# Kernel tuning notes

Hardware: AMD Instinct MI355X
Metric: run time of the kernel (lower is better)

## Reference

```python
import jax, jax.numpy as jnp
import numpy as np

RADIUS = 0.2
K = 32  # num_neighbors


def ball_query(centers, points, radius, k):
    """centers [B,3,M], points [B,3,N] -> int32 indices [B,M,k].
    Matches PointNet++ CUDA semantics: first k points (in original order)
    with squared distance < radius^2; slots beyond the count are filled
    with the first valid index (0 if no point is in the ball)."""
    cn = jnp.sum(centers * centers, axis=1)              # [B,M]
    pn = jnp.sum(points * points, axis=1)                # [B,N]
    cross = jnp.einsum('bdm,bdn->bmn', centers, points)  # [B,M,N]
    d2 = cn[:, :, None] + pn[:, None, :] - 2.0 * cross   # [B,M,N]
    valid = d2 < radius * radius
    # stable argsort puts valid indices first, preserving original order
    order = jnp.argsort(jnp.logical_not(valid), axis=-1, stable=True)
    idx = order[..., :k]                                  # [B,M,k]
    count = jnp.sum(valid, axis=-1, keepdims=True)        # [B,M,1]
    fill = idx[..., :1]                                   # first valid (or 0)
    return jnp.where(jnp.arange(k)[None, None, :] < count, idx, fill)


def group(features, idx):
    """features [B,C,N], idx [B,M,K] -> [B,C,M,K]."""
    return jax.vmap(lambda f, i: jnp.take(f, i, axis=1))(features, idx)


def setup_inputs() -> dict:
    key = jax.random.key(0)
    k1, k2, k3, k4 = jax.random.split(key, 4)
    B, N, M, C, CT = 8, 8192, 2048, 64, 64
    return {
        'points_coords': jax.random.uniform(k1, (B, 3, N), dtype=jnp.float32),
        'centers_coords': jax.random.uniform(k2, (B, 3, M), dtype=jnp.float32),
        'temb': jax.random.normal(k3, (B, CT, N), dtype=jnp.float32),
        'points_features': jax.random.normal(k4, (B, C, N), dtype=jnp.float32),
    }


def reference(points_coords, centers_coords, temb, points_features):
    idx = ball_query(centers_coords, points_coords, RADIUS, K)           # [B,M,K]
    neighbor_coords = group(points_coords, idx) - centers_coords[:, :, :, None]  # [B,3,M,K]
    neighbor_features = jnp.concatenate(
        [neighbor_coords, group(points_features, idx)], axis=1)          # [B,3+C,M,K]
    temb_grouped = group(temb, idx)                                      # [B,CT,M,K]
    return neighbor_features, temb_grouped
```

## Files before the change

kernel.cpp:

```cpp
#include <hip/hip_runtime.h>

#define B  8
#define N  8192
#define M  2048
#define C  64
#define CT 64
#define K  32
#define R2 0.04f

__device__ __forceinline__ float rfl(float x) {
    union { float f; int i; } u;
    u.f = x;
    u.i = __builtin_amdgcn_readfirstlane(u.i);
    return u.f;
}

__global__ __launch_bounds__(256) void transpose_kernel(
    const float* __restrict__ points,
    const float* __restrict__ temb,
    const float* __restrict__ feats,
    float* __restrict__ pointsT,
    float* __restrict__ tembT,
    float* __restrict__ featsT)
{
    const int gx = blockIdx.x;
    if (gx < 2048) {
        const int a  = gx >> 10;
        const int tt = gx & 1023;
        const int b  = tt >> 7;
        const int n0 = (tt & 127) << 6;
        const float* src = (a ? temb : feats) + (size_t)b * 64 * N;
        float* dst = (a ? tembT : featsT) + (size_t)b * N * 64;
        __shared__ float lds[64][65];
        const int nl = threadIdx.x & 63;
        const int c0 = threadIdx.x >> 6;
        #pragma unroll
        for (int i = 0; i < 16; ++i) {
            const int c = c0 + i * 4;
            lds[c][nl] = src[(size_t)c * N + n0 + nl];
        }
        __syncthreads();
        #pragma unroll
        for (int i = 0; i < 16; ++i) {
            const int n = c0 + i * 4;
            dst[(size_t)(n0 + n) * 64 + nl] = lds[nl][n];
        }
    } else {
        const int tt = gx - 2048;
        const int b  = tt >> 5;
        const int n  = ((tt & 31) << 8) + threadIdx.x;
        const float* pc = points + (size_t)b * 3 * N;
        float* dst = pointsT + ((size_t)b * N + n) * 4;
        const float px = pc[n];
        const float py = pc[N + n];
        const float pz = pc[2 * N + n];
        dst[0] = px;
        dst[1] = py;
        dst[2] = pz;
        dst[3] = __fadd_rn(__fadd_rn(__fmul_rn(px, px), __fmul_rn(py, py)),
                           __fmul_rn(pz, pz));
    }
}

#define PROC(vv, nn)                                                          \
    do {                                                                      \
        const float cross = __fadd_rn(                                        \
            __fadd_rn(__fmul_rn(cx, (vv).x), __fmul_rn(cy, (vv).y)),          \
            __fmul_rn(cz, (vv).z));                                           \
        const float d2 = __fsub_rn(__fadd_rn(cn, (vv).w),                     \
                                   __fmul_rn(2.0f, cross));                   \
        const bool valid = d2 < R2;                                           \
        const unsigned long long mask = __ballot(valid);                      \
        if (valid) {                                                          \
            const int slot = cnt + __builtin_amdgcn_mbcnt_hi(                 \
                (unsigned)(mask >> 32),                                       \
                __builtin_amdgcn_mbcnt_lo((unsigned)mask, 0));                \
            if (slot < K) snp[slot] = (nn);                                   \
        }                                                                     \
        cnt += (int)__popcll(mask);                                           \
    } while (0)

__global__ __launch_bounds__(256) void fused_kernel(
    const float* __restrict__ pointsT,
    const float* __restrict__ centers,
    const float* __restrict__ tembT,
    const float* __restrict__ featsT,
    float* __restrict__ out1,
    float* __restrict__ out2)
{
    __shared__ int   sn[128];
    __shared__ float tile[128 * 65];
    __shared__ float ctile[3][128];

    const int t = threadIdx.x;
    const int MB4 = M / 4;
    const int b  = blockIdx.x / MB4;
    const int m0 = (blockIdx.x - b * MB4) * 4;
    const size_t base_mk = (size_t)m0 * K;
    const size_t cs = (size_t)M * K;

    {
        const int wv   = t >> 6;
        const int lane = t & 63;
        const int m    = m0 + wv;
        const float cx = rfl(centers[((size_t)b * 3 + 0) * M + m]);
        const float cy = rfl(centers[((size_t)b * 3 + 1) * M + m]);
        const float cz = rfl(centers[((size_t)b * 3 + 2) * M + m]);
        const float cn = rfl(__fadd_rn(
            __fadd_rn(__fmul_rn(cx, cx), __fmul_rn(cy, cy)),
            __fmul_rn(cz, cz)));

        int* snp = &sn[wv * K];
        if (lane == 0) snp[0] = 0;

        const float4* pt4 = (const float4*)(pointsT + (size_t)b * N * 4);
        int cnt = 0;
        float4 va[4], vb[4];
        #pragma unroll
        for (int j = 0; j < 4; ++j) va[j] = pt4[j * 64 + lane];

        for (int g = 0; g < 32; g += 2) {
            if (g + 1 < 32) {
                #pragma unroll
                for (int j = 0; j < 4; ++j)
                    vb[j] = pt4[((g + 1) * 4 + j) * 64 + lane];
            }
            #pragma unroll
            for (int j = 0; j < 4; ++j) PROC(va[j], g * 256 + j * 64 + lane);
            if (cnt >= K || g + 1 >= 32) break;

            if (g + 2 < 32) {
                #pragma unroll
                for (int j = 0; j < 4; ++j)
                    va[j] = pt4[((g + 2) * 4 + j) * 64 + lane];
            }
            #pragma unroll
            for (int j = 0; j < 4; ++j) PROC(vb[j], (g + 1) * 256 + j * 64 + lane);
            if (cnt >= K) break;
        }

        if (lane < K) {
            const int fill = snp[0];
            const int v    = snp[lane];
            snp[lane] = (lane < cnt) ? v : fill;
        }
    }
    __syncthreads();

    const int cq = t & 15;
    const int pl = t >> 4;
    const float* fT = featsT + (size_t)b * N * 64;
    const float* tT = tembT  + (size_t)b * N * 64;

    #pragma unroll
    for (int i = 0; i < 8; ++i) {
        const int p = i * 16 + pl;
        const int n = sn[p];
        const float4 v = *(const float4*)(fT + (size_t)n * 64 + cq * 4);
        float* d = &tile[p * 65 + cq * 4];
        d[0] = v.x; d[1] = v.y; d[2] = v.z; d[3] = v.w;
    }
    __syncthreads();
    {
        const int p   = t & 127;
        const int ch0 = t >> 7;
        float* o = out1 + (size_t)b * 67 * cs + 3 * cs + base_mk + p;
        #pragma unroll
        for (int i = 0; i < 32; ++i) {
            const int c = ch0 + i * 2;
            o[(size_t)c * cs] = tile[p * 65 + c];
        }
    }
    __syncthreads();

    #pragma unroll
    for (int i = 0; i < 8; ++i) {
        const int p = i * 16 + pl;
        const int n = sn[p];
        const float4 v = *(const float4*)(tT + (size_t)n * 64 + cq * 4);
        float* d = &tile[p * 65 + cq * 4];
        d[0] = v.x; d[1] = v.y; d[2] = v.z; d[3] = v.w;
    }
    __syncthreads();
    {
        const int p   = t & 127;
        const int ch0 = t >> 7;
        float* o = out2 + (size_t)b * 64 * cs + base_mk + p;
        #pragma unroll
        for (int i = 0; i < 32; ++i) {
            const int c = ch0 + i * 2;
            o[(size_t)c * cs] = tile[p * 65 + c];
        }
    }

    if (t < 128) {
        const int p = t;
        const int n = sn[p];
        const int m = m0 + (p >> 5);
        const float4 v = *(const float4*)(pointsT + ((size_t)b * N + n) * 4);
        ctile[0][p] = v.x - centers[((size_t)b * 3 + 0) * M + m];
        ctile[1][p] = v.y - centers[((size_t)b * 3 + 1) * M + m];
        ctile[2][p] = v.z - centers[((size_t)b * 3 + 2) * M + m];
    }
    __syncthreads();
    {
        const int c = t >> 7;
        const int p = t & 127;
        out1[((size_t)b * 67 + c) * cs + base_mk + p] = ctile[c][p];
    }
    if (t < 128) {
        out1[((size_t)b * 67 + 2) * cs + base_mk + t] = ctile[2][t];
    }
}

extern "C" void kernel_launch(void* const* d_in, const int* in_sizes, int n_in,
                              void* d_out, int out_size, void* d_ws, size_t ws_size,
                              hipStream_t stream) {
    const float* points  = (const float*)d_in[0];
    const float* centers = (const float*)d_in[1];
    const float* temb    = (const float*)d_in[2];
    const float* feats   = (const float*)d_in[3];

    float* pointsT = (float*)d_ws;
    float* featsT  = pointsT + (size_t)B * N * 4;
    float* tembT   = featsT  + (size_t)B * N * 64;

    float* out1 = (float*)d_out;
    float* out2 = out1 + (size_t)B * (3 + C) * M * K;

    transpose_kernel<<<2304, 256, 0, stream>>>(points, temb, feats,
                                               pointsT, tembT, featsT);
    fused_kernel<<<(B * M) / 4, 256, 0, stream>>>(pointsT, centers, tembT,
                                                  featsT, out1, out2);
}
```

Measured before the change: 326.7 us.

## Split ball query from gather, interleave batches across blocks, use nontemporal stores

Moves the fused ball-query-plus-gather kernel into two kernels: a ball query kernel that writes neighbour indices to workspace, and a gather kernel that reads them back. The gather kernel then has a uniform memory-bound profile and no longer stalls on the serial search. Block indexing now interleaves batches (b = bid & 7) in all kernels, which may spread concurrent blocks across different batches' data. Streaming outputs and transpose loads/stores use nontemporal hints to reduce cache pollution. The cost is an extra launch and an index round trip through global memory.

```diff
diff --git a/kernel.cpp b/kernel.cpp
--- a/kernel.cpp
+++ b/kernel.cpp
@@ -25,10 +25,10 @@
 {
     const int gx = blockIdx.x;
     if (gx < 2048) {
-        const int a  = gx >> 10;
-        const int tt = gx & 1023;
-        const int b  = tt >> 7;
-        const int n0 = (tt & 127) << 6;
+        const int b  = gx & 7;
+        const int r  = gx >> 3;
+        const int a  = r >> 7;
+        const int n0 = (r & 127) << 6;
         const float* src = (a ? temb : feats) + (size_t)b * 64 * N;
         float* dst = (a ? tembT : featsT) + (size_t)b * N * 64;
         __shared__ float lds[64][65];
@@ -37,18 +37,19 @@
         #pragma unroll
         for (int i = 0; i < 16; ++i) {
             const int c = c0 + i * 4;
-            lds[c][nl] = src[(size_t)c * N + n0 + nl];
+            lds[c][nl] = __builtin_nontemporal_load(&src[(size_t)c * N + n0 + nl]);
         }
         __syncthreads();
         #pragma unroll
         for (int i = 0; i < 16; ++i) {
             const int n = c0 + i * 4;
-            dst[(size_t)(n0 + n) * 64 + nl] = lds[nl][n];
+            __builtin_nontemporal_store(lds[nl][n],
+                                        &dst[(size_t)(n0 + n) * 64 + nl]);
         }
     } else {
         const int tt = gx - 2048;
-        const int b  = tt >> 5;
-        const int n  = ((tt & 31) << 8) + threadIdx.x;
+        const int b  = tt & 7;
+        const int n  = ((tt >> 3) << 8) + threadIdx.x;
         const float* pc = points + (size_t)b * 3 * N;
         float* dst = pointsT + ((size_t)b * N + n) * 4;
         const float px = pc[n];
@@ -80,11 +81,69 @@
         cnt += (int)__popcll(mask);                                           \
     } while (0)
 
-__global__ __launch_bounds__(256) void fused_kernel(
+__global__ __launch_bounds__(256) void ballquery_kernel(
+    const float* __restrict__ pointsT,
+    const float* __restrict__ centers,
+    int* __restrict__ idx)
+{
+    __shared__ int sn[128];
+    const int bid = blockIdx.x;
+    const int b   = bid & 7;
+    const int m0  = (bid >> 3) << 2;
+    const int t    = threadIdx.x;
+    const int wv   = t >> 6;
+    const int lane = t & 63;
+    const int m    = m0 + wv;
+
+    const float cx = rfl(centers[((size_t)b * 3 + 0) * M + m]);
+    const float cy = rfl(centers[((size_t)b * 3 + 1) * M + m]);
+    const float cz = rfl(centers[((size_t)b * 3 + 2) * M + m]);
+    const float cn = rfl(__fadd_rn(
+        __fadd_rn(__fmul_rn(cx, cx), __fmul_rn(cy, cy)),
+        __fmul_rn(cz, cz)));
+
+    int* snp = &sn[wv * K];
+    if (lane == 0) snp[0] = 0;
+
+    const float4* pt4 = (const float4*)(pointsT + (size_t)b * N * 4);
+    int cnt = 0;
+    float4 va[4], vb[4];
+    #pragma unroll
+    for (int j = 0; j < 4; ++j) va[j] = pt4[j * 64 + lane];
+
+    for (int g = 0; g < 32; g += 2) {
+        if (g + 1 < 32) {
+            #pragma unroll
+            for (int j = 0; j < 4; ++j)
+                vb[j] = pt4[((g + 1) * 4 + j) * 64 + lane];
+        }
+        #pragma unroll
+        for (int j = 0; j < 4; ++j) PROC(va[j], g * 256 + j * 64 + lane);
+        if (cnt >= K || g + 1 >= 32) break;
+
+        if (g + 2 < 32) {
+            #pragma unroll
+            for (int j = 0; j < 4; ++j)
+                va[j] = pt4[((g + 2) * 4 + j) * 64 + lane];
+        }
+        #pragma unroll
+        for (int j = 0; j < 4; ++j) PROC(vb[j], (g + 1) * 256 + j * 64 + lane);
+        if (cnt >= K) break;
+    }
+
+    if (lane < K) {
+        const int fill = snp[0];
+        const int v    = snp[lane];
+        idx[((size_t)b * M + m) * K + lane] = (lane < cnt) ? v : fill;
+    }
+}
+
+__global__ __launch_bounds__(256) void gather_kernel(
     const float* __restrict__ pointsT,
     const float* __restrict__ centers,
     const float* __restrict__ tembT,
     const float* __restrict__ featsT,
+    const int*   __restrict__ idx,
     float* __restrict__ out1,
     float* __restrict__ out2)
 {
@@ -92,59 +151,14 @@
     __shared__ float tile[128 * 65];
     __shared__ float ctile[3][128];
 
-    const int t = threadIdx.x;
-    const int MB4 = M / 4;
-    const int b  = blockIdx.x / MB4;
-    const int m0 = (blockIdx.x - b * MB4) * 4;
+    const int t   = threadIdx.x;
+    const int bid = blockIdx.x;
+    const int b   = bid & 7;
+    const int m0  = (bid >> 3) << 2;
     const size_t base_mk = (size_t)m0 * K;
     const size_t cs = (size_t)M * K;
 
-    {
-        const int wv   = t >> 6;
-        const int lane = t & 63;
-        const int m    = m0 + wv;
-        const float cx = rfl(centers[((size_t)b * 3 + 0) * M + m]);
-        const float cy = rfl(centers[((size_t)b * 3 + 1) * M + m]);
-        const float cz = rfl(centers[((size_t)b * 3 + 2) * M + m]);
-        const float cn = rfl(__fadd_rn(
-            __fadd_rn(__fmul_rn(cx, cx), __fmul_rn(cy, cy)),
-            __fmul_rn(cz, cz)));
-
-        int* snp = &sn[wv * K];
-        if (lane == 0) snp[0] = 0;
-
-        const float4* pt4 = (const float4*)(pointsT + (size_t)b * N * 4);
-        int cnt = 0;
-        float4 va[4], vb[4];
-        #pragma unroll
-        for (int j = 0; j < 4; ++j) va[j] = pt4[j * 64 + lane];
-
-        for (int g = 0; g < 32; g += 2) {
-            if (g + 1 < 32) {
-                #pragma unroll
-                for (int j = 0; j < 4; ++j)
-                    vb[j] = pt4[((g + 1) * 4 + j) * 64 + lane];
-            }
-            #pragma unroll
-            for (int j = 0; j < 4; ++j) PROC(va[j], g * 256 + j * 64 + lane);
-            if (cnt >= K || g + 1 >= 32) break;
-
-            if (g + 2 < 32) {
-                #pragma unroll
-                for (int j = 0; j < 4; ++j)
-                    va[j] = pt4[((g + 2) * 4 + j) * 64 + lane];
-            }
-            #pragma unroll
-            for (int j = 0; j < 4; ++j) PROC(vb[j], (g + 1) * 256 + j * 64 + lane);
-            if (cnt >= K) break;
-        }
-
-        if (lane < K) {
-            const int fill = snp[0];
-            const int v    = snp[lane];
-            snp[lane] = (lane < cnt) ? v : fill;
-        }
-    }
+    if (t < 128) sn[t] = idx[((size_t)b * M + m0) * K + t];
     __syncthreads();
 
     const int cq = t & 15;
@@ -168,7 +182,7 @@
         #pragma unroll
         for (int i = 0; i < 32; ++i) {
             const int c = ch0 + i * 2;
-            o[(size_t)c * cs] = tile[p * 65 + c];
+            __builtin_nontemporal_store(tile[p * 65 + c], &o[(size_t)c * cs]);
         }
     }
     __syncthreads();
@@ -189,7 +203,7 @@
         #pragma unroll
         for (int i = 0; i < 32; ++i) {
             const int c = ch0 + i * 2;
-            o[(size_t)c * cs] = tile[p * 65 + c];
+            __builtin_nontemporal_store(tile[p * 65 + c], &o[(size_t)c * cs]);
         }
     }
 
@@ -206,10 +220,12 @@
     {
         const int c = t >> 7;
         const int p = t & 127;
-        out1[((size_t)b * 67 + c) * cs + base_mk + p] = ctile[c][p];
+        __builtin_nontemporal_store(ctile[c][p],
+            &out1[((size_t)b * 67 + c) * cs + base_mk + p]);
     }
     if (t < 128) {
-        out1[((size_t)b * 67 + 2) * cs + base_mk + t] = ctile[2][t];
+        __builtin_nontemporal_store(ctile[2][t],
+            &out1[((size_t)b * 67 + 2) * cs + base_mk + t]);
     }
 }
 
@@ -224,12 +240,14 @@
     float* pointsT = (float*)d_ws;
     float* featsT  = pointsT + (size_t)B * N * 4;
     float* tembT   = featsT  + (size_t)B * N * 64;
+    int*   idxws   = (int*)(tembT + (size_t)B * N * 64);
 
     float* out1 = (float*)d_out;
     float* out2 = out1 + (size_t)B * (3 + C) * M * K;
 
     transpose_kernel<<<2304, 256, 0, stream>>>(points, temb, feats,
                                                pointsT, tembT, featsT);
-    fused_kernel<<<(B * M) / 4, 256, 0, stream>>>(pointsT, centers, tembT,
-                                                  featsT, out1, out2);
-}
+    ballquery_kernel<<<(B * M) / 4, 256, 0, stream>>>(pointsT, centers, idxws);
+    gather_kernel<<<(B * M) / 4, 256, 0, stream>>>(pointsT, centers, tembT,
+                                                   featsT, idxws, out1, out2);
+}
```

Result: slower. 335.7 us (+2.8%).

## Split ball query from gather; gather channel rows from LDS instead of transposing

Applied to the files above, without the earlier changes.

Drops the feature and temb transpose pass. The ball query now runs as its own kernel that writes neighbor indices to workspace and stores the relative coordinates directly. A new gather kernel loads two full channel rows (2×N floats) per block into LDS and writes outputs with coalesced vector nontemporal stores, indexing LDS with the saved indices. This removes the transpose traffic and the strided per-channel output writes. In exchange it adds a third launch, an index round-trip through global memory, and a 64KB LDS footprint per block that limits occupancy.

```diff
diff --git a/kernel.cpp b/kernel.cpp
--- a/kernel.cpp
+++ b/kernel.cpp
@@ -8,6 +8,9 @@
 #define K  32
 #define R2 0.04f
 
+typedef __attribute__((ext_vector_type(4))) float f4;
+typedef __attribute__((ext_vector_type(4))) int   i4;
+
 __device__ __forceinline__ float rfl(float x) {
     union { float f; int i; } u;
     u.f = x;
@@ -15,51 +18,22 @@
     return u.f;
 }
 
-__global__ __launch_bounds__(256) void transpose_kernel(
+__global__ __launch_bounds__(256) void prep_points(
     const float* __restrict__ points,
-    const float* __restrict__ temb,
-    const float* __restrict__ feats,
-    float* __restrict__ pointsT,
-    float* __restrict__ tembT,
-    float* __restrict__ featsT)
+    float* __restrict__ pointsT)
 {
-    const int gx = blockIdx.x;
-    if (gx < 2048) {
-        const int a  = gx >> 10;
-        const int tt = gx & 1023;
-        const int b  = tt >> 7;
-        const int n0 = (tt & 127) << 6;
-        const float* src = (a ? temb : feats) + (size_t)b * 64 * N;
-        float* dst = (a ? tembT : featsT) + (size_t)b * N * 64;
-        __shared__ float lds[64][65];
-        const int nl = threadIdx.x & 63;
-        const int c0 = threadIdx.x >> 6;
-        #pragma unroll
-        for (int i = 0; i < 16; ++i) {
-            const int c = c0 + i * 4;
-            lds[c][nl] = src[(size_t)c * N + n0 + nl];
-        }
-        __syncthreads();
-        #pragma unroll
-        for (int i = 0; i < 16; ++i) {
-            const int n = c0 + i * 4;
-            dst[(size_t)(n0 + n) * 64 + nl] = lds[nl][n];
-        }
-    } else {
-        const int tt = gx - 2048;
-        const int b  = tt >> 5;
-        const int n  = ((tt & 31) << 8) + threadIdx.x;
-        const float* pc = points + (size_t)b * 3 * N;
-        float* dst = pointsT + ((size_t)b * N + n) * 4;
-        const float px = pc[n];
-        const float py = pc[N + n];
-        const float pz = pc[2 * N + n];
-        dst[0] = px;
-        dst[1] = py;
-        dst[2] = pz;
-        dst[3] = __fadd_rn(__fadd_rn(__fmul_rn(px, px), __fmul_rn(py, py)),
-                           __fmul_rn(pz, pz));
-    }
+    const int b = blockIdx.x & 7;
+    const int n = ((blockIdx.x >> 3) << 8) + threadIdx.x;
+    const float* pc = points + (size_t)b * 3 * N;
+    float* dst = pointsT + ((size_t)b * N + n) * 4;
+    const float px = pc[n];
+    const float py = pc[N + n];
+    const float pz = pc[2 * N + n];
+    dst[0] = px;
+    dst[1] = py;
+    dst[2] = pz;
+    dst[3] = __fadd_rn(__fadd_rn(__fmul_rn(px, px), __fmul_rn(py, py)),
+                       __fmul_rn(pz, pz));
 }
 
 #define PROC(vv, nn)                                                          \
@@ -80,136 +54,115 @@
         cnt += (int)__popcll(mask);                                           \
     } while (0)
 
-__global__ __launch_bounds__(256) void fused_kernel(
+__global__ __launch_bounds__(256) void ballquery_kernel(
     const float* __restrict__ pointsT,
     const float* __restrict__ centers,
-    const float* __restrict__ tembT,
-    const float* __restrict__ featsT,
+    int* __restrict__ idx,
+    float* __restrict__ out1)
+{
+    __shared__ int sn[128];
+    const int bid = blockIdx.x;
+    const int b   = bid & 7;
+    const int m0  = (bid >> 3) << 2;
+    const int t    = threadIdx.x;
+    const int wv   = t >> 6;
+    const int lane = t & 63;
+    const int m    = m0 + wv;
+
+    const float cx = rfl(centers[((size_t)b * 3 + 0) * M + m]);
+    const float cy = rfl(centers[((size_t)b * 3 + 1) * M + m]);
+    const float cz = rfl(centers[((size_t)b * 3 + 2) * M + m]);
+    const float cn = rfl(__fadd_rn(
+        __fadd_rn(__fmul_rn(cx, cx), __fmul_rn(cy, cy)),
+        __fmul_rn(cz, cz)));
+
+    int* snp = &sn[wv * K];
+    if (lane == 0) snp[0] = 0;
+
+    const float4* pt4 = (const float4*)(pointsT + (size_t)b * N * 4);
+    int cnt = 0;
+    float4 va[4], vb[4];
+    #pragma unroll
+    for (int j = 0; j < 4; ++j) va[j] = pt4[j * 64 + lane];
+
+    for (int g = 0; g < 32; g += 2) {
+        if (g + 1 < 32) {
+            #pragma unroll
+            for (int j = 0; j < 4; ++j)
+                vb[j] = pt4[((g + 1) * 4 + j) * 64 + lane];
+        }
+        #pragma unroll
+        for (int j = 0; j < 4; ++j) PROC(va[j], g * 256 + j * 64 + lane);
+        if (cnt >= K || g + 1 >= 32) break;
+
+        if (g + 2 < 32) {
+            #pragma unroll
+            for (int j = 0; j < 4; ++j)
+                va[j] = pt4[((g + 2) * 4 + j) * 64 + lane];
+        }
+        #pragma unroll
+        for (int j = 0; j < 4; ++j) PROC(vb[j], (g + 1) * 256 + j * 64 + lane);
+        if (cnt >= K) break;
+    }
+
+    if (lane < K) {
+        const int fill = snp[0];
+        const int v    = snp[lane];
+        const int nf   = (lane < cnt) ? v : fill;
+        idx[((size_t)b * M + m) * K + lane] = nf;
+
+        const float4 p = *(const float4*)(pointsT + ((size_t)b * N + nf) * 4);
+        const size_t cs = (size_t)M * K;
+        const size_t o  = (size_t)b * 67 * cs + (size_t)m * K + lane;
+        __builtin_nontemporal_store(p.x - cx, &out1[o]);
+        __builtin_nontemporal_store(p.y - cy, &out1[o + cs]);
+        __builtin_nontemporal_store(p.z - cz, &out1[o + 2 * cs]);
+    }
+}
+
+__global__ __launch_bounds__(512) void gather_kernel(
+    const float* __restrict__ temb,
+    const float* __restrict__ feats,
+    const int*   __restrict__ idx,
     float* __restrict__ out1,
     float* __restrict__ out2)
 {
-    __shared__ int   sn[128];
-    __shared__ float tile[128 * 65];
-    __shared__ float ctile[3][128];
+    __shared__ float row[2 * N];
 
-    const int t = threadIdx.x;
-    const int MB4 = M / 4;
-    const int b  = blockIdx.x / MB4;
-    const int m0 = (blockIdx.x - b * MB4) * 4;
-    const size_t base_mk = (size_t)m0 * K;
-    const size_t cs = (size_t)M * K;
+    const int bid  = blockIdx.x;
+    const int b    = bid & 7;
+    const int slab = bid >> 3;
+    const int tab  = slab >> 5;
+    const int c0   = (slab & 31) * 2;
+    const int t    = threadIdx.x;
 
-    {
-        const int wv   = t >> 6;
-        const int lane = t & 63;
-        const int m    = m0 + wv;
-        const float cx = rfl(centers[((size_t)b * 3 + 0) * M + m]);
-        const float cy = rfl(centers[((size_t)b * 3 + 1) * M + m]);
-        const float cz = rfl(centers[((size_t)b * 3 + 2) * M + m]);
-        const float cn = rfl(__fadd_rn(
-            __fadd_rn(__fmul_rn(cx, cx), __fmul_rn(cy, cy)),
-            __fmul_rn(cz, cz)));
-
-        int* snp = &sn[wv * K];
-        if (lane == 0) snp[0] = 0;
-
-        const float4* pt4 = (const float4*)(pointsT + (size_t)b * N * 4);
-        int cnt = 0;
-        float4 va[4], vb[4];
-        #pragma unroll
-        for (int j = 0; j < 4; ++j) va[j] = pt4[j * 64 + lane];
-
-        for (int g = 0; g < 32; g += 2) {
-            if (g + 1 < 32) {
-                #pragma unroll
-                for (int j = 0; j < 4; ++j)
-                    vb[j] = pt4[((g + 1) * 4 + j) * 64 + lane];
-            }
-            #pragma unroll
-            for (int j = 0; j < 4; ++j) PROC(va[j], g * 256 + j * 64 + lane);
-            if (cnt >= K || g + 1 >= 32) break;
-
-            if (g + 2 < 32) {
-                #pragma unroll
-                for (int j = 0; j < 4; ++j)
-                    va[j] = pt4[((g + 2) * 4 + j) * 64 + lane];
-            }
-            #pragma unroll
-            for (int j = 0; j < 4; ++j) PROC(vb[j], (g + 1) * 256 + j * 64 + lane);
-            if (cnt >= K) break;
-        }
-
-        if (lane < K) {
-            const int fill = snp[0];
-            const int v    = snp[lane];
-            snp[lane] = (lane < cnt) ? v : fill;
-        }
-    }
+    const f4* src4 = (const f4*)((tab ? temb : feats)
+                                 + ((size_t)b * 64 + c0) * N);
+    f4* lds4 = (f4*)row;
+    #pragma unroll
+    for (int i = 0; i < 8; ++i)
+        lds4[i * 512 + t] = __builtin_nontemporal_load(&src4[i * 512 + t]);
     __syncthreads();
 
-    const int cq = t & 15;
-    const int pl = t >> 4;
-    const float* fT = featsT + (size_t)b * N * 64;
-    const float* tT = tembT  + (size_t)b * N * 64;
+    const size_t cs = (size_t)M * K;
+    float* o0 = tab ? (out2 + ((size_t)b * 64 + c0) * cs)
+                    : (out1 + ((size_t)b * 67 + 3 + c0) * cs);
+    f4* o0v = (f4*)o0;
+    f4* o1v = (f4*)(o0 + cs);
+    const i4* idx4 = (const i4*)(idx + (size_t)b * M * K);
 
-    #pragma unroll
-    for (int i = 0; i < 8; ++i) {
-        const int p = i * 16 + pl;
-        const int n = sn[p];
-        const float4 v = *(const float4*)(fT + (size_t)n * 64 + cq * 4);
-        float* d = &tile[p * 65 + cq * 4];
-        d[0] = v.x; d[1] = v.y; d[2] = v.z; d[3] = v.w;
-    }
-    __syncthreads();
-    {
-        const int p   = t & 127;
-        const int ch0 = t >> 7;
-        float* o = out1 + (size_t)b * 67 * cs + 3 * cs + base_mk + p;
-        #pragma unroll
-        for (int i = 0; i < 32; ++i) {
-            const int c = ch0 + i * 2;
-            o[(size_t)c * cs] = tile[p * 65 + c];
-        }
-    }
-    __syncthreads();
-
-    #pragma unroll
-    for (int i = 0; i < 8; ++i) {
-        const int p = i * 16 + pl;
-        const int n = sn[p];
-        const float4 v = *(const float4*)(tT + (size_t)n * 64 + cq * 4);
-        float* d = &tile[p * 65 + cq * 4];
-        d[0] = v.x; d[1] = v.y; d[2] = v.z; d[3] = v.w;
-    }
-    __syncthreads();
-    {
-        const int p   = t & 127;
-        const int ch0 = t >> 7;
-        float* o = out2 + (size_t)b * 64 * cs + base_mk + p;
-        #pragma unroll
-        for (int i = 0; i < 32; ++i) {
-            const int c = ch0 + i * 2;
-            o[(size_t)c * cs] = tile[p * 65 + c];
-        }
-    }
-
-    if (t < 128) {
-        const int p = t;
-        const int n = sn[p];
-        const int m = m0 + (p >> 5);
-        const float4 v = *(const float4*)(pointsT + ((size_t)b * N + n) * 4);
-        ctile[0][p] = v.x - centers[((size_t)b * 3 + 0) * M + m];
-        ctile[1][p] = v.y - centers[((size_t)b * 3 + 1) * M + m];
-        ctile[2][p] = v.z - centers[((size_t)b * 3 + 2) * M + m];
-    }
-    __syncthreads();
-    {
-        const int c = t >> 7;
-        const int p = t & 127;
-        out1[((size_t)b * 67 + c) * cs + base_mk + p] = ctile[c][p];
-    }
-    if (t < 128) {
-        out1[((size_t)b * 67 + 2) * cs + base_mk + t] = ctile[2][t];
+    i4 nn = idx4[t];
+    for (int it = 0; it < 32; ++it) {
+        const int q = it * 512 + t;
+        const i4 cur = nn;
+        if (it < 31) nn = idx4[q + 512];
+        f4 v0, v1;
+        v0.x = row[cur.x];     v0.y = row[cur.y];
+        v0.z = row[cur.z];     v0.w = row[cur.w];
+        v1.x = row[N + cur.x]; v1.y = row[N + cur.y];
+        v1.z = row[N + cur.z]; v1.w = row[N + cur.w];
+        __builtin_nontemporal_store(v0, &o0v[q]);
+        __builtin_nontemporal_store(v1, &o1v[q]);
     }
 }
 
@@ -222,14 +175,14 @@
     const float* feats   = (const float*)d_in[3];
 
     float* pointsT = (float*)d_ws;
-    float* featsT  = pointsT + (size_t)B * N * 4;
-    float* tembT   = featsT  + (size_t)B * N * 64;
+    int*   idxws   = (int*)(pointsT + (size_t)B * N * 4);
 
     float* out1 = (float*)d_out;
     float* out2 = out1 + (size_t)B * (3 + C) * M * K;
 
-    transpose_kernel<<<2304, 256, 0, stream>>>(points, temb, feats,
-                                               pointsT, tembT, featsT);
-    fused_kernel<<<(B * M) / 4, 256, 0, stream>>>(pointsT, centers, tembT,
-                                                  featsT, out1, out2);
+    prep_points<<<(B * N) / 256, 256, 0, stream>>>(points, pointsT);
+    ballquery_kernel<<<(B * M) / 4, 256, 0, stream>>>(pointsT, centers,
+                                                      idxws, out1);
+    gather_kernel<<<B * 2 * 32, 512, 0, stream>>>(temb, feats, idxws,
+                                                  out1, out2);
 }
```

Result: no change. 324.5 us (-0.7%).
